# Performance work log

Measured on AMD Instinct MI355X. Metric: run time of the kernel, lower is better.

## Reference

```python
import jax, jax.numpy as jnp
import numpy as np

NUM_GROUPS = 32
EPS = 1e-5


def group_norm(x, w, b):
    # x: [B, C, H, W]
    B, C, H, W = x.shape
    xg = x.reshape(B, NUM_GROUPS, C // NUM_GROUPS, H, W)
    mean = jnp.mean(xg, axis=(2, 3, 4), keepdims=True)
    var = jnp.var(xg, axis=(2, 3, 4), keepdims=True)
    xg = (xg - mean) * jax.lax.rsqrt(var + EPS)
    xn = xg.reshape(B, C, H, W)
    return xn * w[None, :, None, None] + b[None, :, None, None]


def conv1x1(x, w, b):
    # x: [B, C, H, W], w: [O, C], b: [O]
    return jnp.einsum('bchw,oc->bohw', x, w) + b[None, :, None, None]


def setup_inputs() -> dict:
    key = jax.random.key(0)
    ks = jax.random.split(key, 10)
    C = 512
    x = jax.random.normal(ks[0], (4, C, 64, 64), dtype=jnp.float32)
    s = 1.0 / np.sqrt(C)
    return {
        'x': x,
        'gn_w': jnp.ones((C,), jnp.float32),
        'gn_b': jnp.zeros((C,), jnp.float32),
        'q_w': jax.random.normal(ks[1], (C, C), jnp.float32) * s,
        'q_b': jax.random.normal(ks[2], (C,), jnp.float32) * 0.01,
        'k_w': jax.random.normal(ks[3], (C, C), jnp.float32) * s,
        'k_b': jax.random.normal(ks[4], (C,), jnp.float32) * 0.01,
        'v_w': jax.random.normal(ks[5], (C, C), jnp.float32) * s,
        'v_b': jax.random.normal(ks[6], (C,), jnp.float32) * 0.01,
        'p_w': jax.random.normal(ks[7], (C, C), jnp.float32) * s,
        'p_b': jax.random.normal(ks[8], (C,), jnp.float32) * 0.01,
    }


def reference(x, gn_w, gn_b, q_w, q_b, k_w, k_b, v_w, v_b, p_w, p_b):
    h_ = group_norm(x, gn_w, gn_b)
    q = conv1x1(h_, q_w, q_b)
    k = conv1x1(h_, k_w, k_b)
    v = conv1x1(h_, v_w, v_b)
    b, c, h, w = q.shape
    n = h * w
    q = q.reshape(b, c, n).transpose(0, 2, 1)   # [b, n, c]
    k = k.reshape(b, c, n)                       # [b, c, n]
    scores = jnp.einsum('bic,bcj->bij', q, k) * (c ** -0.5)  # [b, n, n]
    attn = jax.nn.softmax(scores, axis=-1)
    v = v.reshape(b, c, n)                       # [b, c, n]
    # h_[b,c,i] = sum_j v[b,c,j] * attn[b,i,j]
    h_out = jnp.einsum('bcj,bij->bci', v, attn).reshape(b, c, h, w)
    return x + conv1x1(h_out, p_w, p_b)
```

## Files before the change

### kernel.cpp

```cpp
#include <hip/hip_runtime.h>
#include <hip/hip_bf16.h>
#include <stdint.h>

#define AS1 __attribute__((address_space(1)))
#define AS3 __attribute__((address_space(3)))

typedef unsigned short ushort_t;
typedef __attribute__((ext_vector_type(8))) short short8;
typedef __attribute__((ext_vector_type(4))) float floatx4;
typedef __attribute__((ext_vector_type(16))) float floatx16;
typedef __attribute__((ext_vector_type(2))) unsigned int uint2v;

__device__ __forceinline__ ushort_t f2b(float f) {
    union { float f; unsigned int i; } x; x.f = f;
    unsigned int r = x.i + 0x7fffu + ((x.i >> 16) & 1u);
    return (ushort_t)(r >> 16);
}
__device__ __forceinline__ float b2f(ushort_t u) {
    union { unsigned int i; float f; } x; x.i = ((unsigned int)u) << 16; return x.f;
}
__device__ __forceinline__ void gl2lds16(const void* g, void* l) {
    __builtin_amdgcn_global_load_lds(
        (const AS1 unsigned int*)g,
        (AS3 unsigned int*)l,
        16, 0, 0);
}
__device__ __forceinline__ void plswap(unsigned& a, unsigned& b) {
#if __has_builtin(__builtin_amdgcn_permlane32_swap)
    uint2v r = __builtin_amdgcn_permlane32_swap(a, b, false, false);
    a = r.x; b = r.y;
#else
    asm volatile("v_permlane32_swap_b32 %0, %1" : "+v"(a), "+v"(b));
#endif
}

static constexpr int CCH = 512;
static constexpr int NSP = 4096;
static constexpr int NG  = 32;

__global__ __launch_bounds__(256) void gn_stats(const float* __restrict__ x,
                                                float* __restrict__ mean,
                                                float* __restrict__ rstd) {
    const long base = (long)blockIdx.x * 65536;
    const int t = threadIdx.x;
    float s1 = 0.f, s2 = 0.f;
    for (int i = t * 8; i < 65536; i += 256 * 8) {
        float4 a = *(const float4*)(x + base + i);
        float4 b = *(const float4*)(x + base + i + 4);
        s1 += a.x + a.y + a.z + a.w + b.x + b.y + b.z + b.w;
        s2 += a.x * a.x + a.y * a.y + a.z * a.z + a.w * a.w
            + b.x * b.x + b.y * b.y + b.z * b.z + b.w * b.w;
    }
#pragma unroll
    for (int o = 32; o; o >>= 1) { s1 += __shfl_xor(s1, o, 64); s2 += __shfl_xor(s2, o, 64); }
    __shared__ float r1[4], r2[4];
    const int lane = t & 63, wave = t >> 6;
    if (!lane) { r1[wave] = s1; r2[wave] = s2; }
    __syncthreads();
    if (!t) {
        float S1 = r1[0] + r1[1] + r1[2] + r1[3];
        float S2 = r2[0] + r2[1] + r2[2] + r2[3];
        float mu = S1 * (1.f / 65536.f);
        float var = S2 * (1.f / 65536.f) - mu * mu;
        mean[blockIdx.x] = mu;
        rstd[blockIdx.x] = rsqrtf(var + 1e-5f);
    }
}

__global__ __launch_bounds__(256) void w_to_bf16(const float* __restrict__ q,
                                                 const float* __restrict__ k,
                                                 const float* __restrict__ v,
                                                 const float* __restrict__ p,
                                                 const float* __restrict__ qb,
                                                 ushort_t* __restrict__ out,
                                                 float* __restrict__ sqb) {
    const float scl = 0.044194173824159216f;
    const float* srcs[4] = { q, k, v, p };
    const float* s = srcs[blockIdx.y];
    const float m = (blockIdx.y == 0) ? scl : 1.f;
    const long i = ((long)blockIdx.x * 256 + threadIdx.x) * 4;
    float4 f = *(const float4*)(s + i);
    ushort_t o[4] __attribute__((aligned(8)));
    o[0] = f2b(f.x * m); o[1] = f2b(f.y * m); o[2] = f2b(f.z * m); o[3] = f2b(f.w * m);
    *(ushort4*)(out + (long)blockIdx.y * 262144 + i) = *(ushort4*)o;
    if (blockIdx.y == 0 && blockIdx.x == 0 && threadIdx.x < 128) {
        const int j = threadIdx.x * 4;
        float4 b = *(const float4*)(qb + j);
        sqb[j] = b.x * scl; sqb[j + 1] = b.y * scl; sqb[j + 2] = b.z * scl; sqb[j + 3] = b.w * scl;
    }
}

__global__ __launch_bounds__(256) void norm_transpose(const float* __restrict__ x,
                                                      const float* __restrict__ gw,
                                                      const float* __restrict__ gb,
                                                      const float* __restrict__ mean,
                                                      const float* __restrict__ rstd,
                                                      ushort_t* __restrict__ ht) {
    __shared__ ushort_t tile[64 * 65];
    const int b = blockIdx.z, c0 = blockIdx.y * 64, n0 = blockIdx.x * 64;
    const int t = threadIdx.x;
    const float* xb = x + ((long)b * CCH + c0) * NSP + n0;
#pragma unroll
    for (int p = 0; p < 2; ++p) {
        int li = p * 2048 + t * 8;
        int cl = li >> 6, nl = li & 63;
        int c = c0 + cl, g = c >> 4;
        float mu = mean[b * NG + g], rs = rstd[b * NG + g];
        float w  = gw[c] * rs;
        float bb = gb[c] - mu * w;
        float4 a = *(const float4*)(xb + (long)cl * NSP + nl);
        float4 d = *(const float4*)(xb + (long)cl * NSP + nl + 4);
        float f[8] = { a.x, a.y, a.z, a.w, d.x, d.y, d.z, d.w };
#pragma unroll
        for (int j = 0; j < 8; ++j) tile[cl * 65 + nl + j] = f2b(f[j] * w + bb);
    }
    __syncthreads();
#pragma unroll
    for (int p = 0; p < 2; ++p) {
        int li = p * 2048 + t * 8;
        int nl = li >> 6, cl = li & 63;
        ushort_t v[8] __attribute__((aligned(16)));
#pragma unroll
        for (int j = 0; j < 8; ++j) v[j] = tile[(cl + j) * 65 + nl];
        *(uint4*)(ht + ((long)b * NSP + n0 + nl) * CCH + c0 + cl) = *(uint4*)v;
    }
}

template <int BIAS, int OUTF32, int RES>
__global__ __launch_bounds__(256, 2) void gemm_tn(
    const ushort_t* __restrict__ A, int lda, long sA,
    const ushort_t* __restrict__ B, int ldb, long sB,
    void* __restrict__ Cp, int ldc, long sC,
    const float* __restrict__ bias,
    const float* __restrict__ resid, long sR,
    float scale, int K) {
    __shared__ short As[128 * 32];
    __shared__ short Bs[128 * 32];
    const int t = threadIdx.x;
    const int lane = t & 63, wave = t >> 6;
    const long bz = blockIdx.z;
    const int m0 = blockIdx.y * 128, n0 = blockIdx.x * 128;

    const ushort_t* Ab = A + bz * sA + (long)(m0 + (t >> 2)) * lda + (t & 3) * 8;
    const ushort_t* Bb = B + bz * sB + (long)(n0 + (t >> 2)) * ldb + (t & 3) * 8;
    short* la = As + t * 8;
    short* lb = Bs + t * 8;

    const int wm = (wave & 1) * 64, wn = (wave >> 1) * 64;
    const int lm = lane & 15, lk = (lane >> 4) * 8;
    const short* pa = As + (wm + lm) * 32 + lk;
    const short* pb = Bs + (wn + lm) * 32 + lk;

    floatx4 acc[4][4];
#pragma unroll
    for (int i = 0; i < 4; ++i)
#pragma unroll
        for (int j = 0; j < 4; ++j) acc[i][j] = (floatx4){0.f, 0.f, 0.f, 0.f};

    for (int k0 = 0; k0 < K; k0 += 32) {
        __syncthreads();
        gl2lds16(Ab, la);
        gl2lds16(Ab + 64 * (long)lda, la + 64 * 32);
        gl2lds16(Bb, lb);
        gl2lds16(Bb + 64 * (long)ldb, lb + 64 * 32);
        Ab += 32; Bb += 32;
        __builtin_amdgcn_s_waitcnt(0);
        __syncthreads();
        short8 af[4], bfr[4];
#pragma unroll
        for (int i = 0; i < 4; ++i) af[i]  = *(const short8*)(pa + i * 16 * 32);
#pragma unroll
        for (int i = 0; i < 4; ++i) bfr[i] = *(const short8*)(pb + i * 16 * 32);
#pragma unroll
        for (int mi = 0; mi < 4; ++mi)
#pragma unroll
            for (int ni = 0; ni < 4; ++ni)
                acc[mi][ni] = __builtin_amdgcn_mfma_f32_16x16x32_bf16(af[mi], bfr[ni], acc[mi][ni], 0, 0, 0);
    }

    const int row4 = (lane >> 4) * 4;
    const int ncol = lane & 15;
#pragma unroll
    for (int mi = 0; mi < 4; ++mi) {
#pragma unroll
        for (int ni = 0; ni < 4; ++ni) {
            const int n = n0 + wn + ni * 16 + ncol;
            float bn = (BIAS == 2) ? bias[n] : 0.f;
#pragma unroll
            for (int r = 0; r < 4; ++r) {
                const int m = m0 + wm + mi * 16 + row4 + r;
                float v = acc[mi][ni][r] * scale;
                if (BIAS == 1) v += bias[m];
                if (BIAS == 2) v += bn;
                if (RES) v += resid[bz * sR + (long)m * ldc + n];
                const long idx = bz * sC + (long)m * ldc + n;
                if (OUTF32) ((float*)Cp)[idx] = v;
                else        ((ushort_t*)Cp)[idx] = f2b(v);
            }
        }
    }
}

__global__ __launch_bounds__(256, 1) void flash_attn(const ushort_t* __restrict__ Qt,
                                                     const ushort_t* __restrict__ Kt,
                                                     const ushort_t* __restrict__ V,
                                                     ushort_t* __restrict__ pO0,
                                                     ushort_t* __restrict__ pO1,
                                                     float* __restrict__ ml) {
    __shared__ short Klds[2 * 16384];
    __shared__ short Vlds[2 * 16384];
    const int t = threadIdx.x;
    const int lane = t & 63, wave = t >> 6;
    const int l31 = lane & 31, hi = lane >> 5;
    const int blk = blockIdx.x;
    const int xcd = blk & 7;
    const int bb = xcd >> 1;
    const int split = xcd & 1;
    const int rows0 = (blk >> 3) * 128 + wave * 32;
    const int j_lo = split * 2048;

    const ushort_t* Qb = Qt + ((long)bb * NSP + rows0 + l31) * CCH + hi * 8;
    short8 qf[32];
#pragma unroll
    for (int s = 0; s < 32; ++s) qf[s] = *(const short8*)(Qb + s * 16);

    floatx16 acc[16];
#pragma unroll
    for (int i = 0; i < 16; ++i)
        acc[i] = (floatx16){0.f,0.f,0.f,0.f,0.f,0.f,0.f,0.f,0.f,0.f,0.f,0.f,0.f,0.f,0.f,0.f};
    float lsum = 0.f;

    const ushort_t* KtB = Kt + (long)bb * NSP * CCH;
    const ushort_t* Vb  = V + (long)bb * NSP * CCH;

#define STAGE_K(buf, J0)                                                          \
    {                                                                             \
        short* kb_ = Klds + (buf) * 16384;                                        \
        _Pragma("unroll")                                                         \
        for (int i_ = 0; i_ < 8; ++i_) {                                          \
            const int ch_ = i_ * 256 + t;                                         \
            const int jr_ = ch_ >> 6, m_ = ch_ & 63;                              \
            const int ms_ = m_ ^ (jr_ & 15);                                      \
            gl2lds16(KtB + (long)((J0) + jr_) * CCH + ms_ * 8, kb_ + ch_ * 8);    \
        }                                                                         \
    }
#define STAGE_V(buf, J0)                                                          \
    {                                                                             \
        short* vb_ = Vlds + (buf) * 16384;                                        \
        _Pragma("unroll")                                                         \
        for (int i_ = 0; i_ < 8; ++i_) {                                          \
            const int g_ = i_ * 256 + t;                                          \
            const int d_ = g_ >> 2, mv_ = g_ & 3;                                 \
            const int js_ = (mv_ ^ ((d_ >> 1) & 3)) * 8;                          \
            gl2lds16(Vb + (long)d_ * NSP + (J0) + js_, vb_ + g_ * 8);             \
        }                                                                         \
    }

    STAGE_K(0, j_lo);
    STAGE_V(0, j_lo);
    __builtin_amdgcn_s_waitcnt(0);
    __syncthreads();

    const int exr = (l31 & 15) ^ hi;
    const short* kroot = Klds + l31 * 512;
    const int cv = (l31 >> 1) & 3;
    const int voff0 = l31 * 32 + ((hi ^ cv) << 3);
    const int voff1 = l31 * 32 + (((2 + hi) ^ cv) << 3);

    int j0 = j_lo;
    for (int tile = 0; tile < 64; ++tile) {
        const int cur = tile & 1;
        if (tile + 1 < 64) {
            STAGE_K(cur ^ 1, j0 + 32);
            STAGE_V(cur ^ 1, j0 + 32);
        }
        const short* kp = kroot + cur * 16384;

        floatx16 sE = (floatx16){0.f,0.f,0.f,0.f,0.f,0.f,0.f,0.f,0.f,0.f,0.f,0.f,0.f,0.f,0.f,0.f};
        floatx16 sO = sE;
#pragma unroll
        for (int s2 = 0; s2 < 16; ++s2) {
            short8 k0 = *(const short8*)(kp + (((4 * s2)     ^ exr) << 3));
            short8 k1 = *(const short8*)(kp + (((4 * s2 + 2) ^ exr) << 3));
            sE = __builtin_amdgcn_mfma_f32_32x32x16_bf16(k0, qf[2 * s2],     sE, 0, 0, 0);
            sO = __builtin_amdgcn_mfma_f32_32x32x16_bf16(k1, qf[2 * s2 + 1], sO, 0, 0, 0);
        }

        float pv_[16];
#pragma unroll
        for (int r = 0; r < 16; ++r) { pv_[r] = __expf(sE[r] + sO[r] - 12.f); lsum += pv_[r]; }
        unsigned pk[8];
#pragma unroll
        for (int g = 0; g < 4; ++g) {
            asm("v_cvt_pk_bf16_f32 %0, %1, %2" : "=v"(pk[2 * g])     : "v"(pv_[4 * g]),     "v"(pv_[4 * g + 1]));
            asm("v_cvt_pk_bf16_f32 %0, %1, %2" : "=v"(pk[2 * g + 1]) : "v"(pv_[4 * g + 2]), "v"(pv_[4 * g + 3]));
        }
        plswap(pk[0], pk[2]);
        plswap(pk[1], pk[3]);
        plswap(pk[4], pk[6]);
        plswap(pk[5], pk[7]);
        union { unsigned u[4]; short8 s8; } uA, uB;
        uA.u[0] = pk[0]; uA.u[1] = pk[1]; uA.u[2] = pk[2]; uA.u[3] = pk[3];
        uB.u[0] = pk[4]; uB.u[1] = pk[5]; uB.u[2] = pk[6]; uB.u[3] = pk[7];
        const short8 PA0 = uA.s8;
        const short8 PA1 = uB.s8;

        const short* vp0 = Vlds + cur * 16384 + voff0;
        const short* vp1 = Vlds + cur * 16384 + voff1;
#pragma unroll
        for (int dt = 0; dt < 16; ++dt) {
            short8 v0 = *(const short8*)(vp0 + dt * 1024);
            acc[dt] = __builtin_amdgcn_mfma_f32_32x32x16_bf16(PA0, v0, acc[dt], 0, 0, 0);
        }
#pragma unroll
        for (int dt = 0; dt < 16; ++dt) {
            short8 v1 = *(const short8*)(vp1 + dt * 1024);
            acc[dt] = __builtin_amdgcn_mfma_f32_32x32x16_bf16(PA1, v1, acc[dt], 0, 0, 0);
        }
        __builtin_amdgcn_s_waitcnt(0);
        __syncthreads();
        j0 += 32;
    }
#undef STAGE_K
#undef STAGE_V

    const float lt = lsum + __shfl_xor(lsum, 32, 64);
    ushort_t* pOut = (split ? pO1 : pO0) + ((long)bb * NSP + rows0) * CCH;
#pragma unroll
    for (int dt = 0; dt < 16; ++dt)
#pragma unroll
        for (int r = 0; r < 16; ++r) {
            const int rl = (r & 3) + 8 * (r >> 2) + 4 * hi;
            pOut[(long)rl * CCH + dt * 32 + l31] = f2b(acc[dt][r]);
        }
    if (hi == 0) {
        ml[(long)split * 4 * NSP + (long)bb * NSP + rows0 + l31] = lt;
    }
}

__global__ __launch_bounds__(256) void merge_splits(ushort_t* __restrict__ pO0,
                                                    const ushort_t* __restrict__ pO1,
                                                    const float* __restrict__ ml) {
    const long f = ((long)blockIdx.x * 256 + threadIdx.x) * 8;
    const long row = f >> 9;
    const float inv = 1.f / (ml[row] + ml[(long)4 * NSP + row]);
    uint4 u0 = *(const uint4*)(pO0 + f);
    uint4 u1 = *(const uint4*)(pO1 + f);
    const unsigned int* a = (const unsigned int*)&u0;
    const unsigned int* b = (const unsigned int*)&u1;
    ushort_t out[8] __attribute__((aligned(16)));
#pragma unroll
    for (int i = 0; i < 4; ++i) {
        float x0 = __uint_as_float(a[i] << 16), y0 = __uint_as_float(a[i] & 0xffff0000u);
        float x1 = __uint_as_float(b[i] << 16), y1 = __uint_as_float(b[i] & 0xffff0000u);
        out[2 * i]     = f2b((x0 + x1) * inv);
        out[2 * i + 1] = f2b((y0 + y1) * inv);
    }
    *(uint4*)(pO0 + f) = *(uint4*)out;
}

extern "C" void kernel_launch(void* const* d_in, const int* in_sizes, int n_in,
                              void* d_out, int out_size, void* d_ws, size_t ws_size,
                              hipStream_t stream) {
    const float* x   = (const float*)d_in[0];
    const float* gnw = (const float*)d_in[1];
    const float* gnb = (const float*)d_in[2];
    const float* qw  = (const float*)d_in[3];
    const float* qb  = (const float*)d_in[4];
    const float* kw  = (const float*)d_in[5];
    const float* kb  = (const float*)d_in[6];
    const float* vw  = (const float*)d_in[7];
    const float* vb  = (const float*)d_in[8];
    const float* pw  = (const float*)d_in[9];
    const float* pb  = (const float*)d_in[10];
    float* out = (float*)d_out;
    (void)in_sizes; (void)n_in; (void)out_size; (void)ws_size;

    const long E = (long)NSP * CCH;
    char* ws = (char*)d_ws;
    float*    mean = (float*)ws;
    float*    rstd = (float*)(ws + 512);
    ushort_t* wb   = (ushort_t*)(ws + 1024);
    float*    sqb  = (float*)(wb + 4 * 262144);
    float*    ml   = sqb + 512;
    ushort_t* ht   = (ushort_t*)(ml + 2 * 4 * NSP);
    ushort_t* Kt   = ht + 4 * E;
    ushort_t* V    = Kt + 4 * E;
    ushort_t* Qt   = V  + 4 * E;
    ushort_t* hOT  = Qt + 4 * E;
    ushort_t* qwb = wb, *kwb = wb + 262144, *vwb = wb + 2 * 262144, *pwb = wb + 3 * 262144;

    gn_stats<<<128, 256, 0, stream>>>(x, mean, rstd);
    w_to_bf16<<<dim3(256, 4), 256, 0, stream>>>(qw, kw, vw, pw, qb, wb, sqb);
    norm_transpose<<<dim3(64, 8, 4), 256, 0, stream>>>(x, gnw, gnb, mean, rstd, ht);
    gemm_tn<2, 0, 0><<<dim3(4, 32, 4), 256, 0, stream>>>(ht, 512, E, qwb, 512, 0, Qt, 512, E, sqb, nullptr, 0, 1.f, 512);
    gemm_tn<2, 0, 0><<<dim3(4, 32, 4), 256, 0, stream>>>(ht, 512, E, kwb, 512, 0, Kt, 512, E, kb, nullptr, 0, 1.f, 512);
    gemm_tn<1, 0, 0><<<dim3(32, 4, 4), 256, 0, stream>>>(vwb, 512, 0, ht, 512, E, V, 4096, E, vb, nullptr, 0, 1.f, 512);
    flash_attn<<<256, 256, 0, stream>>>(Qt, Kt, V, hOT, ht, ml);
    merge_splits<<<4096, 256, 0, stream>>>(hOT, ht, ml);
    gemm_tn<1, 1, 1><<<dim3(32, 4, 4), 256, 0, stream>>>(pwb, 512, 0, hOT, 512, E,
                                                         out, 4096, E, pb, x, E, 1.f, 512);
}
```

Baseline: 390.2 us.

## Software-pipeline QK^T of next tile with PV of current tile in attention loop

Restructures the attention loop so the score MFMA for tile j+1 is computed while the PV MFMAs for tile j run, with K prefetched two tiles ahead and V one tile ahead. The softmax/pack step now uses scores from the previous iteration, so the exp work is decoupled from the score MFMA chain that feeds it. This aims to hide the exp/pack latency and the MFMA dependency stalls between the two matmuls. In exchange the score accumulation becomes a single serial chain instead of two interleaved ones, register pressure rises, and there is an extra prologue and epilogue.

```diff
diff --git a/kernel.cpp b/kernel.cpp
--- a/kernel.cpp
+++ b/kernel.cpp
@@ -256,8 +256,30 @@
         }                                                                         \
     }
 
+#define SOFTMAX_PACK(sS, PA0, PA1)                                                \
+    {                                                                             \
+        float pv_[16];                                                            \
+        _Pragma("unroll")                                                         \
+        for (int r = 0; r < 16; ++r) { pv_[r] = __expf((sS)[r] - 12.f); lsum += pv_[r]; } \
+        unsigned pk[8];                                                           \
+        _Pragma("unroll")                                                         \
+        for (int g = 0; g < 4; ++g) {                                             \
+            asm("v_cvt_pk_bf16_f32 %0, %1, %2" : "=v"(pk[2 * g])     : "v"(pv_[4 * g]),     "v"(pv_[4 * g + 1])); \
+            asm("v_cvt_pk_bf16_f32 %0, %1, %2" : "=v"(pk[2 * g + 1]) : "v"(pv_[4 * g + 2]), "v"(pv_[4 * g + 3])); \
+        }                                                                         \
+        plswap(pk[0], pk[2]);                                                     \
+        plswap(pk[1], pk[3]);                                                     \
+        plswap(pk[4], pk[6]);                                                     \
+        plswap(pk[5], pk[7]);                                                     \
+        union { unsigned u[4]; short8 s8; } uA_, uB_;                             \
+        uA_.u[0] = pk[0]; uA_.u[1] = pk[1]; uA_.u[2] = pk[2]; uA_.u[3] = pk[3];   \
+        uB_.u[0] = pk[4]; uB_.u[1] = pk[5]; uB_.u[2] = pk[6]; uB_.u[3] = pk[7];   \
+        (PA0) = uA_.s8; (PA1) = uB_.s8;                                           \
+    }
+
     STAGE_K(0, j_lo);
     STAGE_V(0, j_lo);
+    STAGE_K(1, j_lo + 32);
     __builtin_amdgcn_s_waitcnt(0);
     __syncthreads();
 
@@ -267,62 +289,62 @@
     const int voff0 = l31 * 32 + ((hi ^ cv) << 3);
     const int voff1 = l31 * 32 + (((2 + hi) ^ cv) << 3);
 
+    floatx16 sS = (floatx16){0.f,0.f,0.f,0.f,0.f,0.f,0.f,0.f,0.f,0.f,0.f,0.f,0.f,0.f,0.f,0.f};
+#pragma unroll
+    for (int s2 = 0; s2 < 16; ++s2) {
+        short8 k0 = *(const short8*)(kroot + (((4 * s2)     ^ exr) << 3));
+        short8 k1 = *(const short8*)(kroot + (((4 * s2 + 2) ^ exr) << 3));
+        sS = __builtin_amdgcn_mfma_f32_32x32x16_bf16(k0, qf[2 * s2],     sS, 0, 0, 0);
+        sS = __builtin_amdgcn_mfma_f32_32x32x16_bf16(k1, qf[2 * s2 + 1], sS, 0, 0, 0);
+    }
+    __syncthreads();
+
     int j0 = j_lo;
-    for (int tile = 0; tile < 64; ++tile) {
-        const int cur = tile & 1;
-        if (tile + 1 < 64) {
-            STAGE_K(cur ^ 1, j0 + 32);
-            STAGE_V(cur ^ 1, j0 + 32);
-        }
-        const short* kp = kroot + cur * 16384;
-
-        floatx16 sE = (floatx16){0.f,0.f,0.f,0.f,0.f,0.f,0.f,0.f,0.f,0.f,0.f,0.f,0.f,0.f,0.f,0.f};
-        floatx16 sO = sE;
-#pragma unroll
-        for (int s2 = 0; s2 < 16; ++s2) {
-            short8 k0 = *(const short8*)(kp + (((4 * s2)     ^ exr) << 3));
-            short8 k1 = *(const short8*)(kp + (((4 * s2 + 2) ^ exr) << 3));
-            sE = __builtin_amdgcn_mfma_f32_32x32x16_bf16(k0, qf[2 * s2],     sE, 0, 0, 0);
-            sO = __builtin_amdgcn_mfma_f32_32x32x16_bf16(k1, qf[2 * s2 + 1], sO, 0, 0, 0);
-        }
-
-        float pv_[16];
-#pragma unroll
-        for (int r = 0; r < 16; ++r) { pv_[r] = __expf(sE[r] + sO[r] - 12.f); lsum += pv_[r]; }
-        unsigned pk[8];
-#pragma unroll
-        for (int g = 0; g < 4; ++g) {
-            asm("v_cvt_pk_bf16_f32 %0, %1, %2" : "=v"(pk[2 * g])     : "v"(pv_[4 * g]),     "v"(pv_[4 * g + 1]));
-            asm("v_cvt_pk_bf16_f32 %0, %1, %2" : "=v"(pk[2 * g + 1]) : "v"(pv_[4 * g + 2]), "v"(pv_[4 * g + 3]));
-        }
-        plswap(pk[0], pk[2]);
-        plswap(pk[1], pk[3]);
-        plswap(pk[4], pk[6]);
-        plswap(pk[5], pk[7]);
-        union { unsigned u[4]; short8 s8; } uA, uB;
-        uA.u[0] = pk[0]; uA.u[1] = pk[1]; uA.u[2] = pk[2]; uA.u[3] = pk[3];
-        uB.u[0] = pk[4]; uB.u[1] = pk[5]; uB.u[2] = pk[6]; uB.u[3] = pk[7];
-        const short8 PA0 = uA.s8;
-        const short8 PA1 = uB.s8;
-
+    for (int tile = 0; tile < 63; ++tile) {
+        const int cur = tile & 1, nxt = cur ^ 1;
+        if (tile < 62) STAGE_K(cur, j0 + 64);
+        STAGE_V(nxt, j0 + 32);
+
+        short8 PA0, PA1;
+        SOFTMAX_PACK(sS, PA0, PA1);
+
+        const short* kp  = kroot + nxt * 16384;
         const short* vp0 = Vlds + cur * 16384 + voff0;
         const short* vp1 = Vlds + cur * 16384 + voff1;
-#pragma unroll
-        for (int dt = 0; dt < 16; ++dt) {
-            short8 v0 = *(const short8*)(vp0 + dt * 1024);
-            acc[dt] = __builtin_amdgcn_mfma_f32_32x32x16_bf16(PA0, v0, acc[dt], 0, 0, 0);
+        floatx16 nS = (floatx16){0.f,0.f,0.f,0.f,0.f,0.f,0.f,0.f,0.f,0.f,0.f,0.f,0.f,0.f,0.f,0.f};
+#pragma unroll
+        for (int i = 0; i < 16; ++i) {
+            short8 k0 = *(const short8*)(kp + (((4 * i)     ^ exr) << 3));
+            short8 v0 = *(const short8*)(vp0 + i * 1024);
+            nS = __builtin_amdgcn_mfma_f32_32x32x16_bf16(k0, qf[2 * i], nS, 0, 0, 0);
+            acc[i] = __builtin_amdgcn_mfma_f32_32x32x16_bf16(PA0, v0, acc[i], 0, 0, 0);
+            short8 k1 = *(const short8*)(kp + (((4 * i + 2) ^ exr) << 3));
+            short8 v1 = *(const short8*)(vp1 + i * 1024);
+            nS = __builtin_amdgcn_mfma_f32_32x32x16_bf16(k1, qf[2 * i + 1], nS, 0, 0, 0);
+            acc[i] = __builtin_amdgcn_mfma_f32_32x32x16_bf16(PA1, v1, acc[i], 0, 0, 0);
         }
-#pragma unroll
-        for (int dt = 0; dt < 16; ++dt) {
-            short8 v1 = *(const short8*)(vp1 + dt * 1024);
-            acc[dt] = __builtin_amdgcn_mfma_f32_32x32x16_bf16(PA1, v1, acc[dt], 0, 0, 0);
-        }
+        sS = nS;
         __builtin_amdgcn_s_waitcnt(0);
         __syncthreads();
         j0 += 32;
     }
+
+    {
+        short8 PA0, PA1;
+        SOFTMAX_PACK(sS, PA0, PA1);
+        const short* vp0 = Vlds + 16384 + voff0;
+        const short* vp1 = Vlds + 16384 + voff1;
+#pragma unroll
+        for (int i = 0; i < 16; ++i) {
+            short8 v0 = *(const short8*)(vp0 + i * 1024);
+            acc[i] = __builtin_amdgcn_mfma_f32_32x32x16_bf16(PA0, v0, acc[i], 0, 0, 0);
+            short8 v1 = *(const short8*)(vp1 + i * 1024);
+            acc[i] = __builtin_amdgcn_mfma_f32_32x32x16_bf16(PA1, v1, acc[i], 0, 0, 0);
+        }
+    }
 #undef STAGE_K
 #undef STAGE_V
+#undef SOFTMAX_PACK
 
     const float lt = lsum + __shfl_xor(lsum, 32, 64);
     ushort_t* pOut = (split ? pO1 : pO0) + ((long)bb * NSP + rows0) * CCH;
```

Result: faster. 375.5 us (-3.8%).
